# Performance work log

Hardware: AMD Instinct MI355X
Metric: run time of the kernel (lower is better)

## Reference

```python
import jax, jax.numpy as jnp
import numpy as np
from functools import partial

IMG, P, C, E, DEPTH, H, FE, NCLS = 224, 16, 3, 768, 12, 12, 4, 1000
B = 32
NP = (IMG // P) ** 2          # 196 patches
N = NP + 1                    # +cls token
HD = E // H                   # 64
FF = FE * E                   # 3072
EPS = 1e-5


def setup_inputs() -> dict:
    key = jax.random.key(0)
    ks = iter(jax.random.split(key, 32))
    r = lambda shape, s=0.02: (jax.random.normal(next(ks), shape, jnp.float32) * s)
    inp = {
        "x": jax.random.normal(next(ks), (B, C, IMG, IMG), jnp.float32),
        "conv_w": r((E, C, P, P)),              # OIHW
        "conv_b": r((E,)),
        "cls_token": r((1, 1, E)),
        "pos_emb": r((1, N, E)),
        # stacked per-layer params; Linear weights stored as [in, out]
        "Wq": r((DEPTH, E, E)), "Wk": r((DEPTH, E, E)), "Wv": r((DEPTH, E, E)),
        "Wo": r((DEPTH, E, E)), "bo": r((DEPTH, E)),
        "ln1_g": jnp.ones((DEPTH, E)), "ln1_b": jnp.zeros((DEPTH, E)),
        "W1": r((DEPTH, E, FF)), "b1": r((DEPTH, FF)),
        "W2": r((DEPTH, FF, E)), "b2": r((DEPTH, E)),
        "ln2_g": jnp.ones((DEPTH, E)), "ln2_b": jnp.zeros((DEPTH, E)),
        "head_g": jnp.ones((E,)), "head_b": jnp.zeros((E,)),
        "head_W": r((E, NCLS)), "head_bias": r((NCLS,)),
    }
    return inp


def _ln(x, g, b):
    m = jnp.mean(x, axis=-1, keepdims=True)
    v = jnp.var(x, axis=-1, keepdims=True)
    return (x - m) * jax.lax.rsqrt(v + EPS) * g + b


def _block(h, p):
    Wq, Wk, Wv, Wo, bo, g1, bn1, W1, b1, W2, b2, g2, bn2 = p
    b, n, _ = h.shape
    q = (h @ Wq).reshape(b, n, H, HD)
    k = (h @ Wk).reshape(b, n, H, HD)
    v = (h @ Wv).reshape(b, n, H, HD)
    # NOTE: original scales by sqrt(embed_size), not sqrt(head_dim)
    energy = jnp.einsum("bqhd,bkhd->bhqk", q, k) / jnp.sqrt(jnp.float32(E))
    attn = jax.nn.softmax(energy, axis=-1)
    out = jnp.einsum("bhqk,bkhd->bqhd", attn, v).reshape(b, n, E)
    out = out @ Wo + bo
    x = _ln(out + h, g1, bn1)
    f = jax.nn.relu(x @ W1 + b1) @ W2 + b2
    return _ln(f + x, g2, bn2), None


def reference(x, conv_w, conv_b, cls_token, pos_emb, Wq, Wk, Wv, Wo, bo,
              ln1_g, ln1_b, W1, b1, W2, b2, ln2_g, ln2_b,
              head_g, head_b, head_W, head_bias):
    # patch embedding: strided conv == non-overlapping patch projection
    h = jax.lax.conv_general_dilated(
        x, conv_w, window_strides=(P, P), padding="VALID",
        dimension_numbers=("NCHW", "OIHW", "NCHW"))
    h = h + conv_b[None, :, None, None]
    h = h.reshape(B, E, NP).transpose(0, 2, 1)          # [B, NP, E]
    cls = jnp.broadcast_to(cls_token, (B, 1, E))
    h = jnp.concatenate([cls, h], axis=1) + pos_emb      # [B, N, E]
    params = (Wq, Wk, Wv, Wo, bo, ln1_g, ln1_b, W1, b1, W2, b2, ln2_g, ln2_b)
    h, _ = jax.lax.scan(_block, h, params)
    cls_final = h[:, 0]
    return _ln(cls_final, head_g, head_b) @ head_W + head_bias
```

## Files before the change

### kernel.cpp

```cpp
#include <hip/hip_runtime.h>

#define NTOK 197
#define BATCH 32
#define ROWS (BATCH*NTOK)
#define EMB 768
#define FFDIM 3072
#define NHEAD 12
#define HDIM 64
#define NPAD 224

typedef __bf16 bf16x8_t __attribute__((ext_vector_type(8)));
typedef float f32x4 __attribute__((ext_vector_type(4)));
typedef unsigned short u16;

__device__ __forceinline__ u16 f2b(float f) {
  union { float f; unsigned int u; } v; v.f = f;
  unsigned int r = v.u + 0x7fffu + ((v.u >> 16) & 1u);
  return (u16)(r >> 16);
}
__device__ __forceinline__ void gload16(const void* g, void* l) {
  __builtin_amdgcn_global_load_lds((const __attribute__((address_space(1))) void*)g,
                                   (__attribute__((address_space(3))) void*)l, 16, 0, 0);
}
__device__ __forceinline__ float wred_sum(float v) {
#pragma unroll
  for (int o = 32; o > 0; o >>= 1) v += __shfl_xor(v, o);
  return v;
}

__device__ __forceinline__ void xcd_swz(int& bx, int& by) {
  const int gx = gridDim.x;
  const int nwg = gx * gridDim.y;
  const int orig = by * gx + bx;
  const int q = nwg >> 3, r = nwg & 7;
  const int xcd = orig & 7, idx = orig >> 3;
  const int wg = (xcd < r ? xcd * (q + 1) : r * (q + 1) + (xcd - r) * q) + idx;
  by = wg / gx; bx = wg % gx;
}

template <bool HAS_BIAS, bool RELU, bool ADD_RES, bool OUT_BF16>
__global__ __launch_bounds__(256)
void gemm_bt(const u16* __restrict__ A, const u16* __restrict__ Bt, void* __restrict__ C,
             const float* __restrict__ bias, const float* __restrict__ res,
             int M, int N, int K) {
  __shared__ __align__(16) char lds[2][16384];
  const int tid = threadIdx.x;
  const int lane = tid & 63;
  const int wid = tid >> 6;
  const int wm = wid >> 1, wn = wid & 1;
  int bxs = blockIdx.x, bys = blockIdx.y;
  xcd_swz(bxs, bys);
  const int bm = bys * 128, bn = bxs * 128;
  const int r15 = lane & 15, khi = lane >> 4;

  f32x4 acc[4][4] = {};
  const int nk = K >> 5;

  auto stage = [&](int buf, int kt) {
    const int k0 = kt * 32 + khi * 8;
#pragma unroll
    for (int i = 0; i < 4; ++i) {
      int s = wid * 4 + i;
      char* ldst = &lds[buf][s * 1024];
      const u16* g;
      if (s < 8) {
        int row = bm + s * 16 + r15; if (row >= M) row = M - 1;
        g = A + (size_t)row * K + k0;
      } else {
        int row = bn + (s - 8) * 16 + r15;
        g = Bt + (size_t)row * K + k0;
      }
      gload16(g, ldst);
    }
  };

  stage(0, 0);
  __syncthreads();
  for (int kt = 0; kt < nk; ++kt) {
    const int cur = kt & 1;
    if (kt + 1 < nk) stage(cur ^ 1, kt + 1);
    bf16x8_t a[4], b[4];
#pragma unroll
    for (int mt = 0; mt < 4; ++mt)
      a[mt] = *(const bf16x8_t*)&lds[cur][(wm * 4 + mt) * 1024 + lane * 16];
#pragma unroll
    for (int nt = 0; nt < 4; ++nt)
      b[nt] = *(const bf16x8_t*)&lds[cur][8192 + (wn * 4 + nt) * 1024 + lane * 16];
#pragma unroll
    for (int mt = 0; mt < 4; ++mt)
#pragma unroll
      for (int nt = 0; nt < 4; ++nt)
        acc[mt][nt] = __builtin_amdgcn_mfma_f32_16x16x32_bf16(a[mt], b[nt], acc[mt][nt], 0, 0, 0);
    __syncthreads();
  }

#pragma unroll
  for (int mt = 0; mt < 4; ++mt) {
#pragma unroll
    for (int nt = 0; nt < 4; ++nt) {
      const int col = bn + wn * 64 + nt * 16 + r15;
      float bv = 0.f;
      if (HAS_BIAS) bv = bias[col];
#pragma unroll
      for (int j = 0; j < 4; ++j) {
        const int row = bm + wm * 64 + mt * 16 + khi * 4 + j;
        if (row < M) {
          float v = acc[mt][nt][j] + bv;
          if (ADD_RES) v += res[(size_t)row * N + col];
          if (RELU) v = v > 0.f ? v : 0.f;
          if (OUT_BF16) ((u16*)C)[(size_t)row * N + col] = f2b(v);
          else          ((float*)C)[(size_t)row * N + col] = v;
        }
      }
    }
  }
}

template <bool HAS_BIAS, bool RELU, bool OUT_BF16>
__global__ __launch_bounds__(512)
void gemm_bt2(const u16* __restrict__ A, const u16* __restrict__ Bt, void* __restrict__ C,
              const float* __restrict__ bias, int M, int N, int K) {
  __shared__ __align__(16) char lds[2][24576];
  const int tid = threadIdx.x;
  const int lane = tid & 63;
  const int wid = tid >> 6;
  const int wm = wid >> 1, wn = wid & 1;
  int bxs = blockIdx.x, bys = blockIdx.y;
  xcd_swz(bxs, bys);
  const int bm = bys * 256, bn = bxs * 128;
  const int r15 = lane & 15, khi = lane >> 4;

  f32x4 acc[4][4] = {};
  const int nk = K >> 5;

  auto stage = [&](int buf, int kt) {
    const int k0 = kt * 32 + khi * 8;
#pragma unroll
    for (int i = 0; i < 3; ++i) {
      int s = wid * 3 + i;
      char* ldst = &lds[buf][s * 1024];
      const u16* g;
      if (s < 16) {
        int row = bm + s * 16 + r15; if (row >= M) row = M - 1;
        g = A + (size_t)row * K + k0;
      } else {
        int row = bn + (s - 16) * 16 + r15;
        g = Bt + (size_t)row * K + k0;
      }
      gload16(g, ldst);
    }
  };

  stage(0, 0);
  stage(1, 1);
  for (int kt = 0; kt < nk; ++kt) {
    const int cur = kt & 1;
    if (kt + 1 < nk) { asm volatile("s_waitcnt vmcnt(3)" ::: "memory"); }
    else             { asm volatile("s_waitcnt vmcnt(0)" ::: "memory"); }
    __builtin_amdgcn_sched_barrier(0);
    __builtin_amdgcn_s_barrier();
    bf16x8_t a[4], b[4];
#pragma unroll
    for (int mt = 0; mt < 4; ++mt)
      a[mt] = *(const bf16x8_t*)&lds[cur][(wm * 4 + mt) * 1024 + lane * 16];
#pragma unroll
    for (int nt = 0; nt < 4; ++nt)
      b[nt] = *(const bf16x8_t*)&lds[cur][16384 + (wn * 4 + nt) * 1024 + lane * 16];
#pragma unroll
    for (int mt = 0; mt < 4; ++mt)
#pragma unroll
      for (int nt = 0; nt < 4; ++nt)
        acc[mt][nt] = __builtin_amdgcn_mfma_f32_16x16x32_bf16(a[mt], b[nt], acc[mt][nt], 0, 0, 0);
    asm volatile("s_waitcnt lgkmcnt(0)" ::: "memory");
    __builtin_amdgcn_sched_barrier(0);
    __builtin_amdgcn_s_barrier();
    if (kt + 2 < nk) stage(cur, kt + 2);
  }

#pragma unroll
  for (int mt = 0; mt < 4; ++mt) {
#pragma unroll
    for (int nt = 0; nt < 4; ++nt) {
      const int col = bn + wn * 64 + nt * 16 + r15;
      float bv = 0.f;
      if (HAS_BIAS) bv = bias[col];
#pragma unroll
      for (int j = 0; j < 4; ++j) {
        const int row = bm + wm * 64 + mt * 16 + khi * 4 + j;
        if (row < M) {
          float v = acc[mt][nt][j] + bv;
          if (RELU) v = v > 0.f ? v : 0.f;
          if (OUT_BF16) ((u16*)C)[(size_t)row * N + col] = f2b(v);
          else          ((float*)C)[(size_t)row * N + col] = v;
        }
      }
    }
  }
}

template <int NSK>
__global__ __launch_bounds__(256)
void gemm_bt_sk(const u16* __restrict__ A, const u16* __restrict__ Bt,
                float* __restrict__ P0, float* __restrict__ P1, float* __restrict__ P2,
                int M, int N, int K) {
  __shared__ __align__(16) char lds[2][16384];
  const int tid = threadIdx.x;
  const int lane = tid & 63;
  const int wid = tid >> 6;
  const int wm = wid >> 1, wn = wid & 1;
  int bxs = blockIdx.x, bys = blockIdx.y;
  xcd_swz(bxs, bys);
  const int bm = bys * 128, bn = bxs * 128;
  const int r15 = lane & 15, khi = lane >> 4;
  const int Kh = K / NSK;
  const int kbase = blockIdx.z * Kh;
  float* __restrict__ C = (blockIdx.z == 0) ? P0 : (blockIdx.z == 1 ? P1 : P2);

  f32x4 acc[4][4] = {};
  const int nk = Kh >> 5;

  auto stage = [&](int buf, int kt) {
    const int k0 = kbase + kt * 32 + khi * 8;
#pragma unroll
    for (int i = 0; i < 4; ++i) {
      int s = wid * 4 + i;
      char* ldst = &lds[buf][s * 1024];
      const u16* g;
      if (s < 8) {
        int row = bm + s * 16 + r15; if (row >= M) row = M - 1;
        g = A + (size_t)row * K + k0;
      } else {
        int row = bn + (s - 8) * 16 + r15;
        g = Bt + (size_t)row * K + k0;
      }
      gload16(g, ldst);
    }
  };

  stage(0, 0);
  stage(1, 1);
  for (int kt = 0; kt < nk; ++kt) {
    const int cur = kt & 1;
    if (kt + 1 < nk) { asm volatile("s_waitcnt vmcnt(4)" ::: "memory"); }
    else             { asm volatile("s_waitcnt vmcnt(0)" ::: "memory"); }
    __builtin_amdgcn_sched_barrier(0);
    __builtin_amdgcn_s_barrier();
    bf16x8_t a[4], b[4];
#pragma unroll
    for (int mt = 0; mt < 4; ++mt)
      a[mt] = *(const bf16x8_t*)&lds[cur][(wm * 4 + mt) * 1024 + lane * 16];
#pragma unroll
    for (int nt = 0; nt < 4; ++nt)
      b[nt] = *(const bf16x8_t*)&lds[cur][8192 + (wn * 4 + nt) * 1024 + lane * 16];
#pragma unroll
    for (int mt = 0; mt < 4; ++mt)
#pragma unroll
      for (int nt = 0; nt < 4; ++nt)
        acc[mt][nt] = __builtin_amdgcn_mfma_f32_16x16x32_bf16(a[mt], b[nt], acc[mt][nt], 0, 0, 0);
    asm volatile("s_waitcnt lgkmcnt(0)" ::: "memory");
    __builtin_amdgcn_sched_barrier(0);
    __builtin_amdgcn_s_barrier();
    if (kt + 2 < nk) stage(cur, kt + 2);
  }

#pragma unroll
  for (int mt = 0; mt < 4; ++mt) {
#pragma unroll
    for (int nt = 0; nt < 4; ++nt) {
      const int col = bn + wn * 64 + nt * 16 + r15;
#pragma unroll
      for (int j = 0; j < 4; ++j) {
        const int row = bm + wm * 64 + mt * 16 + khi * 4 + j;
        if (row < M) C[(size_t)row * N + col] = acc[mt][nt][j];
      }
    }
  }
}

__global__ __launch_bounds__(256)
void ln_red(const float* __restrict__ P0, const float* __restrict__ P1,
            const float* __restrict__ P2,
            const float* __restrict__ bias, const float* __restrict__ res,
            const float* __restrict__ g, const float* __restrict__ bv,
            float* __restrict__ o32, u16* __restrict__ obf) {
  const int row = blockIdx.x;
  const size_t base = (size_t)row * EMB;
  const int tid = threadIdx.x;
  float vv[3];
#pragma unroll
  for (int c = 0; c < 3; ++c) {
    int e = tid + c * 256;
    vv[c] = P0[base + e] + P1[base + e] + P2[base + e] + bias[e] + res[base + e];
  }
  float s = wred_sum(vv[0] + vv[1] + vv[2]);
  float s2 = wred_sum(vv[0] * vv[0] + vv[1] * vv[1] + vv[2] * vv[2]);
  __shared__ float rs[4], rq[4];
  const int wid = tid >> 6, lane = tid & 63;
  if (lane == 0) { rs[wid] = s; rq[wid] = s2; }
  __syncthreads();
  float S1 = rs[0] + rs[1] + rs[2] + rs[3];
  float S2 = rq[0] + rq[1] + rq[2] + rq[3];
  float mean = S1 * (1.0f / 768.0f);
  float var = S2 * (1.0f / 768.0f) - mean * mean;
  float inv = rsqrtf(var + 1e-5f);
#pragma unroll
  for (int c = 0; c < 3; ++c) {
    int e = tid + c * 256;
    float y = (vv[c] - mean) * inv * g[e] + bv[e];
    o32[base + e] = y;
    obf[base + e] = f2b(y);
  }
}

__global__ void prep_layer(const float* __restrict__ Wq, const float* __restrict__ Wk,
                           const float* __restrict__ Wv, const float* __restrict__ Wo,
                           const float* __restrict__ W1, const float* __restrict__ W2,
                           u16* __restrict__ qkvT, u16* __restrict__ woT,
                           u16* __restrict__ w1T, u16* __restrict__ w2T) {
  __shared__ float tbuf[32][33];
  const int t = blockIdx.x;
  const float* src; u16* dst; int K, N, nt, kt;
  if (t < 2304) {
    int seg = t / 576, r = t % 576;
    nt = r % 24; kt = r / 24; K = 768; N = 768;
    if (seg == 0)      { src = Wq; dst = qkvT; }
    else if (seg == 1) { src = Wk; dst = qkvT + (size_t)768 * 768; }
    else if (seg == 2) { src = Wv; dst = qkvT + (size_t)2 * 768 * 768; }
    else               { src = Wo; dst = woT; }
  } else if (t < 4608) {
    int r = t - 2304; nt = r % 96; kt = r / 96;
    K = 768; N = 3072; src = W1; dst = w1T;
  } else {
    int r = t - 4608; nt = r % 24; kt = r / 24;
    K = 3072; N = 768; src = W2; dst = w2T;
  }
  const int n0 = nt * 32, k0 = kt * 32;
  const int tx = threadIdx.x, ty = threadIdx.y;
#pragma unroll
  for (int i = 0; i < 4; ++i)
    tbuf[ty + i * 8][tx] = src[(size_t)(k0 + ty + i * 8) * N + n0 + tx];
  __syncthreads();
#pragma unroll
  for (int i = 0; i < 4; ++i)
    dst[(size_t)(n0 + ty + i * 8) * K + k0 + tx] = f2b(tbuf[tx][ty + i * 8]);
}

__global__ void convert_bf(const float* __restrict__ s, u16* __restrict__ d, size_t n) {
  size_t i = (size_t)blockIdx.x * 256 + threadIdx.x;
  if (i < n) d[i] = f2b(s[i]);
}

__global__ void transpose_head(const float* __restrict__ src, float* __restrict__ dst) {
  __shared__ float tbuf[32][33];
  const int n0 = blockIdx.x * 32, k0 = blockIdx.y * 32;
  const int tx = threadIdx.x, ty = threadIdx.y;
#pragma unroll
  for (int i = 0; i < 4; ++i) {
    int k = k0 + ty + i * 8, n = n0 + tx;
    if (n < 1000) tbuf[ty + i * 8][tx] = src[(size_t)k * 1000 + n];
  }
  __syncthreads();
#pragma unroll
  for (int i = 0; i < 4; ++i) {
    int n = n0 + ty + i * 8, k = k0 + tx;
    if (n < 1000) dst[(size_t)n * 768 + k] = tbuf[tx][ty + i * 8];
  }
}

__global__ void im2col(const float* __restrict__ x, u16* __restrict__ A) {
  size_t idx = (size_t)blockIdx.x * 256 + threadIdx.x;
  if (idx >= (size_t)6272 * 768) return;
  int k = (int)(idx % 768); size_t row = idx / 768;
  int b = (int)(row / 196), p = (int)(row % 196);
  int py = p / 14, px = p % 14;
  int c = k >> 8, rem = k & 255, ph = rem >> 4, pw = rem & 15;
  float v = x[(((size_t)b * 3 + c) * 224 + (py * 16 + ph)) * 224 + (px * 16 + pw)];
  A[idx] = f2b(v);
}

__global__ void assemble_h0(const float* __restrict__ pout, const float* __restrict__ cls,
                            const float* __restrict__ pos, float* __restrict__ h32,
                            u16* __restrict__ hbf) {
  const int row = blockIdx.x;
  const int b = row / NTOK, n = row % NTOK;
  for (int c = threadIdx.x; c < EMB; c += 256) {
    float v;
    if (n == 0) v = cls[c] + pos[c];
    else v = pout[((size_t)b * 196 + (n - 1)) * EMB + c] + pos[(size_t)n * EMB + c];
    h32[(size_t)row * EMB + c] = v;
    hbf[(size_t)row * EMB + c] = f2b(v);
  }
}

__global__ void build_vT(const u16* __restrict__ qkv, u16* __restrict__ vT) {
  size_t idx = (size_t)blockIdx.x * 256 + threadIdx.x;
  if (idx >= (size_t)384 * HDIM * NPAD) return;
  int nn = (int)(idx % NPAD); size_t t = idx / NPAD;
  int d = (int)(t % HDIM); int bh = (int)(t / HDIM);
  int b = bh / NHEAD, h = bh % NHEAD;
  u16 v = 0;
  if (nn < NTOK) v = qkv[((size_t)b * NTOK + nn) * 2304 + 1536 + h * HDIM + d];
  vT[idx] = v;
}

__global__ __launch_bounds__(256)
void attn_sm(const u16* __restrict__ qkv, u16* __restrict__ P) {
  __shared__ __align__(16) char kf[13 * 2 * 1024];
  __shared__ __align__(16) char qf[2 * 2 * 1024];
  __shared__ float S[32][NPAD];
  const int bh = blockIdx.y;
  const int b = bh / NHEAD, h = bh % NHEAD;
  const int qb = blockIdx.x;
  const int tid = threadIdx.x, lane = tid & 63, wid = tid >> 6;
  const int r15 = lane & 15, khi = lane >> 4;

  const u16* qbase = qkv + (size_t)b * NTOK * 2304 + h * HDIM;
  const u16* kbase = qbase + 768;

  for (int i = wid; i < 26; i += 4) {
    int sub = i >> 1, ks = i & 1;
    int row = sub * 16 + r15; if (row > 196) row = 196;
    gload16(kbase + (size_t)row * 2304 + ks * 32 + khi * 8, &kf[(size_t)i * 1024]);
  }
  {
    int i = wid;
    int sub = i >> 1, ks = i & 1;
    int row = qb * 32 + sub * 16 + r15; if (row > 196) row = 196;
    gload16(qbase + (size_t)row * 2304 + ks * 32 + khi * 8, &qf[(size_t)i * 1024]);
  }
  __syncthreads();

  const float scale = 0.03608439182435161f;
  for (int t = wid; t < 26; t += 4) {
    int qi = t / 13, ki = t % 13;
    f32x4 acc = {};
    bf16x8_t aq0 = *(const bf16x8_t*)&qf[(qi * 2 + 0) * 1024 + lane * 16];
    bf16x8_t aq1 = *(const bf16x8_t*)&qf[(qi * 2 + 1) * 1024 + lane * 16];
    bf16x8_t bk0 = *(const bf16x8_t*)&kf[(ki * 2 + 0) * 1024 + lane * 16];
    bf16x8_t bk1 = *(const bf16x8_t*)&kf[(ki * 2 + 1) * 1024 + lane * 16];
    acc = __builtin_amdgcn_mfma_f32_16x16x32_bf16(aq0, bk0, acc, 0, 0, 0);
    acc = __builtin_amdgcn_mfma_f32_16x16x32_bf16(aq1, bk1, acc, 0, 0, 0);
#pragma unroll
    for (int j = 0; j < 4; ++j) S[qi * 16 + khi * 4 + j][ki * 16 + r15] = acc[j] * scale;
  }
  __syncthreads();

  for (int i = 0; i < 8; ++i) {
    const int r = wid * 8 + i;
    const int q = qb * 32 + r;
    if (q > 196) continue;
    float vals[4]; float m = -1e30f;
#pragma unroll
    for (int c = 0; c < 4; ++c) {
      int col = lane + c * 64;
      float v = (col < NTOK) ? S[r][col] : -1e30f;
      vals[c] = v; m = fmaxf(m, v);
    }
#pragma unroll
    for (int o = 32; o > 0; o >>= 1) m = fmaxf(m, __shfl_xor(m, o));
    float s = 0.f;
#pragma unroll
    for (int c = 0; c < 4; ++c) { float e = __expf(vals[c] - m); vals[c] = e; s += e; }
    s = wred_sum(s);
    float inv = 1.f / s;
    u16* prow = P + ((size_t)bh * NTOK + q) * NPAD;
#pragma unroll
    for (int c = 0; c < 4; ++c) {
      int col = lane + c * 64;
      if (col < NPAD) prow[col] = f2b(vals[c] * inv);
    }
  }
}

__global__ __launch_bounds__(256)
void attn_pv(const u16* __restrict__ P, const u16* __restrict__ vT, u16* __restrict__ out) {
  __shared__ __align__(16) char lds[2][17 * 1024];
  const int bh = blockIdx.x;
  const int b = bh / NHEAD, h = bh % NHEAD;
  const int tid = threadIdx.x, lane = tid & 63, wid = tid >> 6;
  const int r15 = lane & 15, khi = lane >> 4;
  const u16* Pb = P + (size_t)bh * NTOK * NPAD;
  const u16* Vb = vT + (size_t)bh * HDIM * NPAD;

  f32x4 acc[4][4] = {};
  auto stage = [&](int buf, int kt) {
    for (int i = wid; i < 17; i += 4) {
      const u16* g;
      if (i < 13) { int row = i * 16 + r15; if (row > 196) row = 196;
                    g = Pb + (size_t)row * NPAD + kt * 32 + khi * 8; }
      else        { int row = (i - 13) * 16 + r15;
                    g = Vb + (size_t)row * NPAD + kt * 32 + khi * 8; }
      gload16(g, &lds[buf][i * 1024]);
    }
  };
  stage(0, 0);
  __syncthreads();
  for (int kt = 0; kt < 7; ++kt) {
    const int cur = kt & 1;
    if (kt + 1 < 7) stage(cur ^ 1, kt + 1);
    bf16x8_t bb[4];
#pragma unroll
    for (int di = 0; di < 4; ++di)
      bb[di] = *(const bf16x8_t*)&lds[cur][(13 + di) * 1024 + lane * 16];
#pragma unroll
    for (int s = 0; s < 4; ++s) {
      int qi = wid + s * 4;
      if (qi < 13) {
        bf16x8_t a = *(const bf16x8_t*)&lds[cur][qi * 1024 + lane * 16];
#pragma unroll
        for (int di = 0; di < 4; ++di)
          acc[s][di] = __builtin_amdgcn_mfma_f32_16x16x32_bf16(a, bb[di], acc[s][di], 0, 0, 0);
      }
    }
    __syncthreads();
  }
#pragma unroll
  for (int s = 0; s < 4; ++s) {
    int qi = wid + s * 4;
    if (qi >= 13) continue;
#pragma unroll
    for (int di = 0; di < 4; ++di) {
      int col = h * HDIM + di * 16 + r15;
#pragma unroll
      for (int j = 0; j < 4; ++j) {
        int q = qi * 16 + khi * 4 + j;
        if (q < NTOK) out[((size_t)b * NTOK + q) * EMB + col] = f2b(acc[s][di][j]);
      }
    }
  }
}

__global__ __launch_bounds__(256)
void ln_cls(const float* __restrict__ h32, const float* __restrict__ hg,
            const float* __restrict__ hb, float* __restrict__ cls_ln) {
  const int b = blockIdx.x;
  const float* xr = h32 + (size_t)b * NTOK * EMB;
  const int tid = threadIdx.x;
  float v0 = xr[tid], v1 = xr[tid + 256], v2 = xr[tid + 512];
  float s = wred_sum(v0 + v1 + v2);
  float s2 = wred_sum(v0 * v0 + v1 * v1 + v2 * v2);
  __shared__ float rs[4], rq[4];
  const int wid = tid >> 6, lane = tid & 63;
  if (lane == 0) { rs[wid] = s; rq[wid] = s2; }
  __syncthreads();
  float S1 = rs[0] + rs[1] + rs[2] + rs[3];
  float S2 = rq[0] + rq[1] + rq[2] + rq[3];
  float mean = S1 * (1.0f / 768.0f);
  float var = S2 * (1.0f / 768.0f) - mean * mean;
  float inv = rsqrtf(var + 1e-5f);
  cls_ln[(size_t)b * EMB + tid]       = (v0 - mean) * inv * hg[tid]       + hb[tid];
  cls_ln[(size_t)b * EMB + tid + 256] = (v1 - mean) * inv * hg[tid + 256] + hb[tid + 256];
  cls_ln[(size_t)b * EMB + tid + 512] = (v2 - mean) * inv * hg[tid + 512] + hb[tid + 512];
}

__global__ __launch_bounds__(256)
void head2(const float* __restrict__ cls_ln, const float* __restrict__ hWT,
           const float* __restrict__ bias, float* __restrict__ out) {
  __shared__ float t[EMB];
  const int b = blockIdx.y;
  const int tid = threadIdx.x, lane = tid & 63, wid = tid >> 6;
  t[tid] = cls_ln[(size_t)b * EMB + tid];
  t[tid + 256] = cls_ln[(size_t)b * EMB + tid + 256];
  t[tid + 512] = cls_ln[(size_t)b * EMB + tid + 512];
  __syncthreads();
  const int j = blockIdx.x * 4 + wid;
  const float* wr = hWT + (size_t)j * EMB;
  float a = 0.f;
#pragma unroll
  for (int i = 0; i < 12; ++i) {
    int e = lane + i * 64;
    a += t[e] * wr[e];
  }
  a = wred_sum(a);
  if (lane == 0) out[(size_t)b * 1000 + j] = a + bias[j];
}

extern "C" void kernel_launch(void* const* d_in, const int* in_sizes, int n_in,
                              void* d_out, int out_size, void* d_ws, size_t ws_size,
                              hipStream_t stream) {
  const float* x      = (const float*)d_in[0];
  const float* conv_w = (const float*)d_in[1];
  const float* conv_b = (const float*)d_in[2];
  const float* cls    = (const float*)d_in[3];
  const float* pos    = (const float*)d_in[4];
  const float* Wq     = (const float*)d_in[5];
  const float* Wk     = (const float*)d_in[6];
  const float* Wv     = (const float*)d_in[7];
  const float* Wo     = (const float*)d_in[8];
  const float* bo     = (const float*)d_in[9];
  const float* ln1g   = (const float*)d_in[10];
  const float* ln1b   = (const float*)d_in[11];
  const float* W1     = (const float*)d_in[12];
  const float* b1     = (const float*)d_in[13];
  const float* W2     = (const float*)d_in[14];
  const float* b2     = (const float*)d_in[15];
  const float* ln2g   = (const float*)d_in[16];
  const float* ln2b   = (const float*)d_in[17];
  const float* hg     = (const float*)d_in[18];
  const float* hb     = (const float*)d_in[19];
  const float* hW     = (const float*)d_in[20];
  const float* hbias  = (const float*)d_in[21];

  char* ws = (char*)d_ws;
  size_t off = 0;
  auto alloc = [&](size_t bytes) { void* p = ws + off; off += (bytes + 255) & ~(size_t)255; return p; };

  u16*   qkvT = (u16*)alloc((size_t)2304 * 768 * 2);
  u16*   woTl = (u16*)alloc((size_t)768 * 768 * 2);
  u16*   w1Tl = (u16*)alloc((size_t)3072 * 768 * 2);
  u16*   w2Tl = (u16*)alloc((size_t)768 * 3072 * 2);
  u16*   cw   = (u16*)alloc((size_t)768 * 768 * 2);
  float* h32  = (float*)alloc((size_t)ROWS * EMB * 4);
  u16*   hbf  = (u16*)alloc((size_t)ROWS * EMB * 2);
  u16*   qkv  = (u16*)alloc((size_t)ROWS * 2304 * 2);
  char*  big  = (char*)alloc((size_t)384 * NTOK * NPAD * 2 + (size_t)384 * HDIM * NPAD * 2);
  u16*   Pbuf = (u16*)big;
  u16*   vT   = (u16*)(big + (size_t)384 * NTOK * NPAD * 2);
  u16*   mid  = (u16*)big;
  float* pout = (float*)big;
  float* woP0 = (float*)big;
  float* woP1 = (float*)(big + (size_t)ROWS * EMB * 4);
  u16*   att  = (u16*)alloc((size_t)ROWS * EMB * 2);
  u16*   xbf  = att;
  float* ybuf = (float*)alloc((size_t)ROWS * EMB * 4);
  float* x32  = (float*)alloc((size_t)ROWS * EMB * 4);
  float* hWT  = (float*)alloc((size_t)1000 * EMB * 4);
  float* clsl = (float*)alloc((size_t)32 * EMB * 4);
  u16*   Apatch = qkv;
  float* woP2 = ybuf;
  float* f2P0 = (float*)qkv;
  float* f2P1 = ybuf;
  float* f2P2 = h32;

  if (off > ws_size) return;

  convert_bf<<<2304, 256, 0, stream>>>(conv_w, cw, (size_t)768 * 768);
  transpose_head<<<dim3(32, 24), dim3(32, 8), 0, stream>>>(hW, hWT);
  im2col<<<18816, 256, 0, stream>>>(x, Apatch);
  gemm_bt<true, false, false, false><<<dim3(6, 49), 256, 0, stream>>>(Apatch, cw, pout, conv_b, nullptr, 6272, 768, 768);
  assemble_h0<<<ROWS, 256, 0, stream>>>(pout, cls, pos, h32, hbf);

  for (int l = 0; l < 12; ++l) {
    const size_t wo = (size_t)l * 768 * 768;
    prep_layer<<<6912, dim3(32, 8), 0, stream>>>(
        Wq + wo, Wk + wo, Wv + wo, Wo + wo,
        W1 + (size_t)l * 768 * 3072, W2 + (size_t)l * 3072 * 768,
        qkvT, woTl, w1Tl, w2Tl);
    gemm_bt2<false, false, true><<<dim3(18, 25), 512, 0, stream>>>(
        hbf, qkvT, qkv, nullptr, ROWS, 2304, 768);
    build_vT<<<21504, 256, 0, stream>>>(qkv, vT);
    attn_sm<<<dim3(7, 384), 256, 0, stream>>>(qkv, Pbuf);
    attn_pv<<<384, 256, 0, stream>>>(Pbuf, vT, att);
    gemm_bt_sk<3><<<dim3(6, 50, 3), 256, 0, stream>>>(att, woTl, woP0, woP1, woP2, ROWS, 768, 768);
    ln_red<<<ROWS, 256, 0, stream>>>(woP0, woP1, woP2, bo + (size_t)l * 768, h32,
                                     ln1g + (size_t)l * 768, ln1b + (size_t)l * 768, x32, xbf);
    gemm_bt2<true, true, true><<<dim3(24, 25), 512, 0, stream>>>(
        xbf, w1Tl, mid, b1 + (size_t)l * 3072, ROWS, FFDIM, 768);
    gemm_bt_sk<3><<<dim3(6, 50, 3), 256, 0, stream>>>(mid, w2Tl, f2P0, f2P1, f2P2, ROWS, 768, FFDIM);
    ln_red<<<ROWS, 256, 0, stream>>>(f2P0, f2P1, f2P2, b2 + (size_t)l * 768, x32,
                                     ln2g + (size_t)l * 768, ln2b + (size_t)l * 768, h32, hbf);
  }

  ln_cls<<<32, 256, 0, stream>>>(h32, hg, hb, clsl);
  head2<<<dim3(250, 32), 256, 0, stream>>>(clsl, hWT, hbias, (float*)d_out);
}
```

Before: 3.852 ms.

## Fold V transpose into QKV GEMM epilogue and split attn_pv across query blocks

New measurement: 3.949 ms. 2.5% more time.

```diff
diff --git a/kernel.cpp b/kernel.cpp
--- a/kernel.cpp
+++ b/kernel.cpp
@@ -116,10 +116,10 @@
   }
 }
 
-template <bool HAS_BIAS, bool RELU, bool OUT_BF16>
+template <bool HAS_BIAS, bool RELU, bool OUT_BF16, bool VT_FOLD>
 __global__ __launch_bounds__(512)
 void gemm_bt2(const u16* __restrict__ A, const u16* __restrict__ Bt, void* __restrict__ C,
-              const float* __restrict__ bias, int M, int N, int K) {
+              const float* __restrict__ bias, u16* __restrict__ vTp, int M, int N, int K) {
   __shared__ __align__(16) char lds[2][24576];
   const int tid = threadIdx.x;
   const int lane = tid & 63;
@@ -187,11 +187,17 @@
 #pragma unroll
       for (int j = 0; j < 4; ++j) {
         const int row = bm + wm * 64 + mt * 16 + khi * 4 + j;
-        if (row < M) {
-          float v = acc[mt][nt][j] + bv;
-          if (RELU) v = v > 0.f ? v : 0.f;
-          if (OUT_BF16) ((u16*)C)[(size_t)row * N + col] = f2b(v);
-          else          ((float*)C)[(size_t)row * N + col] = v;
+        if (row >= M) continue;
+        float v = acc[mt][nt][j] + bv;
+        if (RELU) v = v > 0.f ? v : 0.f;
+        if (VT_FOLD && col >= 1536) {
+          const int hh = (col - 1536) >> 6, dd = (col - 1536) & 63;
+          const int bb = row / NTOK, nn = row - bb * NTOK;
+          vTp[((size_t)(bb * NHEAD + hh) * HDIM + dd) * NPAD + nn] = f2b(v);
+        } else if (OUT_BF16) {
+          ((u16*)C)[(size_t)row * N + col] = f2b(v);
+        } else {
+          ((float*)C)[(size_t)row * N + col] = v;
         }
       }
     }
@@ -350,6 +356,11 @@
   if (i < n) d[i] = f2b(s[i]);
 }
 
+__global__ void zero_u16(u16* __restrict__ p, size_t n) {
+  size_t i = (size_t)blockIdx.x * 256 + threadIdx.x;
+  if (i < n) p[i] = 0;
+}
+
 __global__ void transpose_head(const float* __restrict__ src, float* __restrict__ dst) {
   __shared__ float tbuf[32][33];
   const int n0 = blockIdx.x * 32, k0 = blockIdx.y * 32;
@@ -392,17 +403,6 @@
   }
 }
 
-__global__ void build_vT(const u16* __restrict__ qkv, u16* __restrict__ vT) {
-  size_t idx = (size_t)blockIdx.x * 256 + threadIdx.x;
-  if (idx >= (size_t)384 * HDIM * NPAD) return;
-  int nn = (int)(idx % NPAD); size_t t = idx / NPAD;
-  int d = (int)(t % HDIM); int bh = (int)(t / HDIM);
-  int b = bh / NHEAD, h = bh % NHEAD;
-  u16 v = 0;
-  if (nn < NTOK) v = qkv[((size_t)b * NTOK + nn) * 2304 + 1536 + h * HDIM + d];
-  vT[idx] = v;
-}
-
 __global__ __launch_bounds__(256)
 void attn_sm(const u16* __restrict__ qkv, u16* __restrict__ P) {
   __shared__ __align__(16) char kf[13 * 2 * 1024];
@@ -473,59 +473,44 @@
 }
 
 __global__ __launch_bounds__(256)
-void attn_pv(const u16* __restrict__ P, const u16* __restrict__ vT, u16* __restrict__ out) {
-  __shared__ __align__(16) char lds[2][17 * 1024];
-  const int bh = blockIdx.x;
+void attn_pv2(const u16* __restrict__ P, const u16* __restrict__ vT, u16* __restrict__ out) {
+  __shared__ __align__(16) char pf[14 * 1024];
+  __shared__ __align__(16) char vf[28 * 1024];
+  const int bh = blockIdx.y, qb = blockIdx.x;
   const int b = bh / NHEAD, h = bh % NHEAD;
   const int tid = threadIdx.x, lane = tid & 63, wid = tid >> 6;
   const int r15 = lane & 15, khi = lane >> 4;
   const u16* Pb = P + (size_t)bh * NTOK * NPAD;
   const u16* Vb = vT + (size_t)bh * HDIM * NPAD;
 
-  f32x4 acc[4][4] = {};
-  auto stage = [&](int buf, int kt) {
-    for (int i = wid; i < 17; i += 4) {
-      const u16* g;
-      if (i < 13) { int row = i * 16 + r15; if (row > 196) row = 196;
-                    g = Pb + (size_t)row * NPAD + kt * 32 + khi * 8; }
-      else        { int row = (i - 13) * 16 + r15;
-                    g = Vb + (size_t)row * NPAD + kt * 32 + khi * 8; }
-      gload16(g, &lds[buf][i * 1024]);
-    }
-  };
-  stage(0, 0);
-  __syncthreads();
-  for (int kt = 0; kt < 7; ++kt) {
-    const int cur = kt & 1;
-    if (kt + 1 < 7) stage(cur ^ 1, kt + 1);
-    bf16x8_t bb[4];
-#pragma unroll
-    for (int di = 0; di < 4; ++di)
-      bb[di] = *(const bf16x8_t*)&lds[cur][(13 + di) * 1024 + lane * 16];
-#pragma unroll
-    for (int s = 0; s < 4; ++s) {
-      int qi = wid + s * 4;
-      if (qi < 13) {
-        bf16x8_t a = *(const bf16x8_t*)&lds[cur][qi * 1024 + lane * 16];
-#pragma unroll
-        for (int di = 0; di < 4; ++di)
-          acc[s][di] = __builtin_amdgcn_mfma_f32_16x16x32_bf16(a, bb[di], acc[s][di], 0, 0, 0);
-      }
-    }
-    __syncthreads();
-  }
-#pragma unroll
-  for (int s = 0; s < 4; ++s) {
-    int qi = wid + s * 4;
-    if (qi >= 13) continue;
-#pragma unroll
-    for (int di = 0; di < 4; ++di) {
-      int col = h * HDIM + di * 16 + r15;
-#pragma unroll
-      for (int j = 0; j < 4; ++j) {
-        int q = qi * 16 + khi * 4 + j;
-        if (q < NTOK) out[((size_t)b * NTOK + q) * EMB + col] = f2b(acc[s][di][j]);
-      }
+  for (int i = wid; i < 42; i += 4) {
+    if (i < 14) {
+      int qsub = i / 7, ksl = i % 7;
+      int row = qb * 32 + qsub * 16 + r15; if (row > 196) row = 196;
+      gload16(Pb + (size_t)row * NPAD + ksl * 32 + khi * 8, &pf[(size_t)i * 1024]);
+    } else {
+      int j = i - 14, dsub = j / 7, ksl = j % 7;
+      gload16(Vb + (size_t)(dsub * 16 + r15) * NPAD + ksl * 32 + khi * 8, &vf[(size_t)j * 1024]);
+    }
+  }
+  __syncthreads();
+
+  const int qsub = wid & 1, dbase = wid >> 1;
+#pragma unroll
+  for (int t = 0; t < 2; ++t) {
+    const int dsub = dbase + t * 2;
+    f32x4 acc = {};
+#pragma unroll
+    for (int ksl = 0; ksl < 7; ++ksl) {
+      bf16x8_t a  = *(const bf16x8_t*)&pf[(size_t)(qsub * 7 + ksl) * 1024 + lane * 16];
+      bf16x8_t bv = *(const bf16x8_t*)&vf[(size_t)(dsub * 7 + ksl) * 1024 + lane * 16];
+      acc = __builtin_amdgcn_mfma_f32_16x16x32_bf16(a, bv, acc, 0, 0, 0);
+    }
+    const int col = h * HDIM + dsub * 16 + r15;
+#pragma unroll
+    for (int j = 0; j < 4; ++j) {
+      int q = qb * 32 + qsub * 16 + khi * 4 + j;
+      if (q < NTOK) out[((size_t)b * NTOK + q) * EMB + col] = f2b(acc[j]);
     }
   }
 }
@@ -613,9 +598,9 @@
   float* h32  = (float*)alloc((size_t)ROWS * EMB * 4);
   u16*   hbf  = (u16*)alloc((size_t)ROWS * EMB * 2);
   u16*   qkv  = (u16*)alloc((size_t)ROWS * 2304 * 2);
-  char*  big  = (char*)alloc((size_t)384 * NTOK * NPAD * 2 + (size_t)384 * HDIM * NPAD * 2);
+  u16*   vT   = (u16*)alloc((size_t)384 * HDIM * NPAD * 2);
+  char*  big  = (char*)alloc(2 * (size_t)ROWS * EMB * 4);
   u16*   Pbuf = (u16*)big;
-  u16*   vT   = (u16*)(big + (size_t)384 * NTOK * NPAD * 2);
   u16*   mid  = (u16*)big;
   float* pout = (float*)big;
   float* woP0 = (float*)big;
@@ -636,6 +621,7 @@
 
   convert_bf<<<2304, 256, 0, stream>>>(conv_w, cw, (size_t)768 * 768);
   transpose_head<<<dim3(32, 24), dim3(32, 8), 0, stream>>>(hW, hWT);
+  zero_u16<<<21504, 256, 0, stream>>>(vT, (size_t)384 * HDIM * NPAD);
   im2col<<<18816, 256, 0, stream>>>(x, Apatch);
   gemm_bt<true, false, false, false><<<dim3(6, 49), 256, 0, stream>>>(Apatch, cw, pout, conv_b, nullptr, 6272, 768, 768);
   assemble_h0<<<ROWS, 256, 0, stream>>>(pout, cls, pos, h32, hbf);
@@ -646,16 +632,15 @@
         Wq + wo, Wk + wo, Wv + wo, Wo + wo,
         W1 + (size_t)l * 768 * 3072, W2 + (size_t)l * 3072 * 768,
         qkvT, woTl, w1Tl, w2Tl);
-    gemm_bt2<false, false, true><<<dim3(18, 25), 512, 0, stream>>>(
-        hbf, qkvT, qkv, nullptr, ROWS, 2304, 768);
-    build_vT<<<21504, 256, 0, stream>>>(qkv, vT);
+    gemm_bt2<false, false, true, true><<<dim3(18, 25), 512, 0, stream>>>(
+        hbf, qkvT, qkv, nullptr, vT, ROWS, 2304, 768);
     attn_sm<<<dim3(7, 384), 256, 0, stream>>>(qkv, Pbuf);
-    attn_pv<<<384, 256, 0, stream>>>(Pbuf, vT, att);
+    attn_pv2<<<dim3(7, 384), 256, 0, stream>>>(Pbuf, vT, att);
     gemm_bt_sk<3><<<dim3(6, 50, 3), 256, 0, stream>>>(att, woTl, woP0, woP1, woP2, ROWS, 768, 768);
     ln_red<<<ROWS, 256, 0, stream>>>(woP0, woP1, woP2, bo + (size_t)l * 768, h32,
                                      ln1g + (size_t)l * 768, ln1b + (size_t)l * 768, x32, xbf);
-    gemm_bt2<true, true, true><<<dim3(24, 25), 512, 0, stream>>>(
-        xbf, w1Tl, mid, b1 + (size_t)l * 3072, ROWS, FFDIM, 768);
+    gemm_bt2<true, true, true, false><<<dim3(24, 25), 512, 0, stream>>>(
+        xbf, w1Tl, mid, b1 + (size_t)l * 3072, nullptr, ROWS, FFDIM, 768);
     gemm_bt_sk<3><<<dim3(6, 50, 3), 256, 0, stream>>>(mid, w2Tl, f2P0, f2P1, f2P2, ROWS, 768, FFDIM);
     ln_red<<<ROWS, 256, 0, stream>>>(f2P0, f2P1, f2P2, b2 + (size_t)l * 768, x32,
                                      ln2g + (size_t)l * 768, ln2b + (size_t)l * 768, h32, hbf);
```
